# Optimization experiments

Hardware: AMD Instinct MI355X
Metric: run time of the kernel (lower is better)

Reference implementation:

```python
import jax, jax.numpy as jnp
import numpy as np

B = 1048576          # batch size
ALPHA1, ALPHA2, ALPHA3 = 1.2566, 1.5, 0.9
S_STAR = 20.0
TAU = 4.0


def _f_matrix(a1, a2, a3):
    # fixed 6x6 dynamics matrix built by the i in {1,2} loop in CBF_Parameters
    f = jnp.zeros((6, 6), jnp.float32)
    f = f.at[2, 1].set(1.0).at[2, 3].set(-1.0)
    f = f.at[3, 1].set(a3).at[3, 2].set(a1).at[3, 3].set(-a2)
    f = f.at[4, 3].set(1.0).at[4, 5].set(-1.0)
    f = f.at[5, 3].set(a3).at[5, 4].set(a1).at[5, 5].set(-a2)
    return f


def setup_inputs() -> dict:
    key = jax.random.key(0)
    ks = jax.random.split(key, 7)
    z = jax.random.normal(ks[0], (B, 6), jnp.float32)
    tilde_vh = jnp.zeros((1,), jnp.float32)  # unused in forward (dead code in source)
    W1 = jax.random.normal(ks[1], (50, 6), jnp.float32) * 0.3
    b1 = jax.random.normal(ks[2], (50,), jnp.float32) * 0.1
    W2 = jax.random.normal(ks[3], (100, 50), jnp.float32) * 0.1
    b2 = jax.random.normal(ks[4], (100,), jnp.float32) * 0.1
    W3 = jax.random.normal(ks[5], (5, 100), jnp.float32) * 0.1
    b3 = jax.random.normal(ks[6], (5,), jnp.float32) * 0.1
    return dict(z=z, tilde_vh=tilde_vh, W1=W1, b1=b1, W2=W2, b2=b2, W3=W3, b3=b3)


def reference(z, tilde_vh, W1, b1, W2, b2, W3, b3):
    # tiny MLP, no activations (faithful to fc3(fc2(fc1(z))))
    u = ((z @ W1.T + b1) @ W2.T + b2) @ W3.T + b3        # (B, 5)
    p1, p2, p3 = u[:, 1], u[:, 2], u[:, 3]

    # faithful: torch reshape (row-major reinterpret), not transpose
    X = z.reshape(6, -1)                                  # (6, B)
    f = _f_matrix(ALPHA1, ALPHA2, ALPHA3)
    fX = f @ X                                            # (6, B)

    # index == 2 constraint (while loop body never runs: delta_b[1]=tau != 0)
    d2 = jnp.zeros(6, jnp.float32).at[1].set(TAU).at[2].set(1.0).at[3].set(-TAU)
    eta1 = X[2] + S_STAR - TAU * (X[3] - X[1])            # (B,)
    bb1 = d2 @ fX + p1 * eta1                             # (B,)

    # index == 3 constraint (while loop runs exactly once: d3[1]==0 -> d3u[1]=tau*alpha3)
    d3 = jnp.zeros(6, jnp.float32).at[3].set(TAU).at[4].set(1.0).at[5].set(-TAU)
    d3u = d3 @ f                                          # one f-multiplication
    eta2a = X[4] + S_STAR - TAU * (X[5] - X[3])           # (B,)
    eta2b = d3u @ X                                       # (B,)
    bb2 = d3u @ fX + p2 * eta2a + p3 * eta2b              # (B,)

    A = jnp.stack([-d2[1], -d3u[1]])                      # (2,) constraint normals
    h = jnp.stack([bb1, bb2], axis=1)                     # (B, 2)

    # per-sample 1-D QP: min 0.25*x^2 - u0*x  s.t. A_i * x <= h_i  (Q = 0.5)
    x_unc = 2.0 * u[:, 0]
    ratios = h / A                                        # (B, 2)
    neg_inf = jnp.float32(-1e30)
    pos_inf = jnp.float32(1e30)
    lb = jnp.max(jnp.where(A < 0, ratios, neg_inf), axis=1)
    ub = jnp.min(jnp.where(A > 0, ratios, pos_inf), axis=1)
    return jnp.clip(x_unc, lb, ub)[:, None]               # (B, 1)
```

## Files before the change

### kernel.cpp

```cpp
#include <hip/hip_runtime.h>

#define ALPHA1 1.2566f
#define ALPHA2 1.5f
#define ALPHA3 0.9f
#define S_STAR 20.0f
#define TAU    4.0f

constexpr int TPB = 256;
constexpr int JPT = 2;
constexpr int JPB = TPB * JPT;

typedef float f32x4 __attribute__((ext_vector_type(4)));
typedef float f32x2 __attribute__((ext_vector_type(2)));

__device__ __forceinline__ f32x4 ntload4(const float* p) {
    return __builtin_nontemporal_load((const f32x4*)p);
}
__device__ __forceinline__ f32x2 ntload2(const float* p) {
    return __builtin_nontemporal_load((const f32x2*)p);
}

__global__ __launch_bounds__(TPB, 8) void fused_kernel(
        const float* __restrict__ z,
        const float* __restrict__ W1, const float* __restrict__ b1,
        const float* __restrict__ W2, const float* __restrict__ b2,
        const float* __restrict__ W3, const float* __restrict__ b3,
        float* __restrict__ out, long long B) {
    __shared__ float W1e[50][8];
    __shared__ float T[100][8];
    __shared__ float Mc[4][8];

    const int tid = threadIdx.x;
    const long long j0 = ((long long)blockIdx.x * TPB + tid) * JPT;

    const f32x4 r0 = ntload4(z + j0 * 6);
    const f32x4 r1 = ntload4(z + j0 * 6 + 4);
    const f32x4 r2 = ntload4(z + j0 * 6 + 8);
    const f32x2 c1 = ntload2(z + 1 * B + j0);
    const f32x2 c2 = ntload2(z + 2 * B + j0);
    const f32x2 c3 = ntload2(z + 3 * B + j0);
    const f32x2 c4 = ntload2(z + 4 * B + j0);
    const f32x2 c5 = ntload2(z + 5 * B + j0);

    if (tid < 50) {
        const float2 a = *(const float2*)(W1 + tid * 6);
        const float2 b = *(const float2*)(W1 + tid * 6 + 2);
        const float2 d = *(const float2*)(W1 + tid * 6 + 4);
        W1e[tid][0] = a.x; W1e[tid][1] = a.y;
        W1e[tid][2] = b.x; W1e[tid][3] = b.y;
        W1e[tid][4] = d.x; W1e[tid][5] = d.y;
        W1e[tid][6] = b1[tid];
    }
    __syncthreads();

    if (tid < 100) {
        float acc[7] = {0.f, 0.f, 0.f, 0.f, 0.f, 0.f, 0.f};
        acc[6] = b2[tid];
        const float2* wrow = (const float2*)(W2 + tid * 50);
        #pragma unroll 5
        for (int hh = 0; hh < 25; ++hh) {
            const float2 w = wrow[hh];
            const int h = 2 * hh;
            #pragma unroll
            for (int k = 0; k < 7; ++k)
                acc[k] = fmaf(w.y, W1e[h + 1][k], fmaf(w.x, W1e[h][k], acc[k]));
        }
        #pragma unroll
        for (int k = 0; k < 7; ++k) T[tid][k] = acc[k];
    }
    __syncthreads();

    if (tid < 28) {
        const int m = tid / 7, k = tid % 7;
        float s = (k == 6) ? b3[m] : 0.f;
        #pragma unroll 10
        for (int i = 0; i < 100; ++i)
            s = fmaf(W3[m * 100 + i], T[i][k], s);
        Mc[m][k] = s;
    }
    __syncthreads();

    const float g1 = TAU * ALPHA3;
    const float g2 = TAU * ALPHA1;
    const float g3 = 1.f - TAU * ALPHA2 - TAU * ALPHA3;
    const float g4 = -TAU * ALPHA1;
    const float g5 = TAU * ALPHA2 - 1.f;
    const float invA1 = -0.25f;
    const float invA2 = -1.f / (TAU * ALPHA3);

    const float zz[12] = {r0.x, r0.y, r0.z, r0.w,
                          r1.x, r1.y, r1.z, r1.w,
                          r2.x, r2.y, r2.z, r2.w};

    f32x2 o;
    #pragma unroll
    for (int r = 0; r < 2; ++r) {
        float u[4];
        #pragma unroll
        for (int m = 0; m < 4; ++m) {
            float s = Mc[m][6];
            #pragma unroll
            for (int k = 0; k < 6; ++k)
                s = fmaf(Mc[m][k], zz[r * 6 + k], s);
            u[m] = s;
        }
        const float x1 = r ? c1.y : c1.x;
        const float x2 = r ? c2.y : c2.x;
        const float x3 = r ? c3.y : c3.x;
        const float x4 = r ? c4.y : c4.x;
        const float x5 = r ? c5.y : c5.x;

        const float fx2 = x1 - x3;
        const float fx3 = ALPHA3 * x1 + ALPHA1 * x2 - ALPHA2 * x3;
        const float fx4 = x3 - x5;
        const float fx5 = ALPHA3 * x3 + ALPHA1 * x4 - ALPHA2 * x5;

        const float eta1 = x2 + S_STAR - TAU * (x3 - x1);
        const float bb1  = (fx2 - TAU * fx3) + u[1] * eta1;

        const float eta2a = x4 + S_STAR - TAU * (x5 - x3);
        const float eta2b = g1 * x1 + g2 * x2 + g3 * x3 + g4 * x4 + g5 * x5;
        const float d3ufX = g2 * fx2 + g3 * fx3 + g4 * fx4 + g5 * fx5;
        const float bb2   = d3ufX + u[2] * eta2a + u[3] * eta2b;

        const float lb = fmaxf(bb1 * invA1, bb2 * invA2);
        const float xu = 2.f * u[0];
        o[r] = fminf(fmaxf(xu, lb), 1e30f);
    }
    __builtin_nontemporal_store(o, (f32x2*)(out + j0));
}

extern "C" void kernel_launch(void* const* d_in, const int* in_sizes, int n_in,
                              void* d_out, int out_size, void* d_ws, size_t ws_size,
                              hipStream_t stream) {
    const float* z  = (const float*)d_in[0];
    const float* W1 = (const float*)d_in[2];
    const float* b1 = (const float*)d_in[3];
    const float* W2 = (const float*)d_in[4];
    const float* b2 = (const float*)d_in[5];
    const float* W3 = (const float*)d_in[6];
    const float* b3 = (const float*)d_in[7];
    float* out = (float*)d_out;

    const long long B = (long long)in_sizes[0] / 6;
    const int blocks = (int)(B / JPB);

    fused_kernel<<<blocks, TPB, 0, stream>>>(z, W1, b1, W2, b2, W3, b3, out, B);
}
```

Before: 105.9 us.

## Drop W1 LDS staging barrier, prefetch W3/b3 to LDS, use regular loads

Removes the first shared-memory staging of W1/b1 and its barrier; threads building the composite weights now read W1 and b1 directly from global memory (uniform addresses, likely scalar loads). Otherwise idle threads preload W3 and b3 into LDS in parallel, so the third-stage reduction reads from LDS instead of global memory. Non-temporal loads and stores of z and out are replaced with ordinary vector accesses, and the column loads are reordered before the row loads. Trade-off: each of the 100 threads reads W1 from global or cache instead of LDS, and cache policy changes for the streaming traffic.

```diff
diff --git a/kernel.cpp b/kernel.cpp
--- a/kernel.cpp
+++ b/kernel.cpp
@@ -13,45 +13,35 @@
 typedef float f32x4 __attribute__((ext_vector_type(4)));
 typedef float f32x2 __attribute__((ext_vector_type(2)));
 
-__device__ __forceinline__ f32x4 ntload4(const float* p) {
-    return __builtin_nontemporal_load((const f32x4*)p);
-}
-__device__ __forceinline__ f32x2 ntload2(const float* p) {
-    return __builtin_nontemporal_load((const f32x2*)p);
-}
-
 __global__ __launch_bounds__(TPB, 8) void fused_kernel(
         const float* __restrict__ z,
         const float* __restrict__ W1, const float* __restrict__ b1,
         const float* __restrict__ W2, const float* __restrict__ b2,
         const float* __restrict__ W3, const float* __restrict__ b3,
         float* __restrict__ out, long long B) {
-    __shared__ float W1e[50][8];
     __shared__ float T[100][8];
+    __shared__ float W3s[400];
+    __shared__ float b3s[4];
     __shared__ float Mc[4][8];
 
     const int tid = threadIdx.x;
     const long long j0 = ((long long)blockIdx.x * TPB + tid) * JPT;
 
-    const f32x4 r0 = ntload4(z + j0 * 6);
-    const f32x4 r1 = ntload4(z + j0 * 6 + 4);
-    const f32x4 r2 = ntload4(z + j0 * 6 + 8);
-    const f32x2 c1 = ntload2(z + 1 * B + j0);
-    const f32x2 c2 = ntload2(z + 2 * B + j0);
-    const f32x2 c3 = ntload2(z + 3 * B + j0);
-    const f32x2 c4 = ntload2(z + 4 * B + j0);
-    const f32x2 c5 = ntload2(z + 5 * B + j0);
+    const f32x2 c1 = *(const f32x2*)(z + 1 * B + j0);
+    const f32x2 c2 = *(const f32x2*)(z + 2 * B + j0);
+    const f32x2 c3 = *(const f32x2*)(z + 3 * B + j0);
+    const f32x2 c4 = *(const f32x2*)(z + 4 * B + j0);
+    const f32x2 c5 = *(const f32x2*)(z + 5 * B + j0);
+    const f32x4 r0 = *(const f32x4*)(z + j0 * 6);
+    const f32x4 r1 = *(const f32x4*)(z + j0 * 6 + 4);
+    const f32x4 r2 = *(const f32x4*)(z + j0 * 6 + 8);
 
-    if (tid < 50) {
-        const float2 a = *(const float2*)(W1 + tid * 6);
-        const float2 b = *(const float2*)(W1 + tid * 6 + 2);
-        const float2 d = *(const float2*)(W1 + tid * 6 + 4);
-        W1e[tid][0] = a.x; W1e[tid][1] = a.y;
-        W1e[tid][2] = b.x; W1e[tid][3] = b.y;
-        W1e[tid][4] = d.x; W1e[tid][5] = d.y;
-        W1e[tid][6] = b1[tid];
+    if (tid >= 128 && tid < 228) {
+        const int i = tid - 128;
+        *(f32x4*)(&W3s[i * 4]) = *(const f32x4*)(W3 + i * 4);
+    } else if (tid >= 228 && tid < 232) {
+        b3s[tid - 228] = b3[tid - 228];
     }
-    __syncthreads();
 
     if (tid < 100) {
         float acc[7] = {0.f, 0.f, 0.f, 0.f, 0.f, 0.f, 0.f};
@@ -62,8 +52,10 @@
             const float2 w = wrow[hh];
             const int h = 2 * hh;
             #pragma unroll
-            for (int k = 0; k < 7; ++k)
-                acc[k] = fmaf(w.y, W1e[h + 1][k], fmaf(w.x, W1e[h][k], acc[k]));
+            for (int k = 0; k < 6; ++k)
+                acc[k] = fmaf(w.y, W1[(h + 1) * 6 + k],
+                          fmaf(w.x, W1[h * 6 + k], acc[k]));
+            acc[6] = fmaf(w.y, b1[h + 1], fmaf(w.x, b1[h], acc[6]));
         }
         #pragma unroll
         for (int k = 0; k < 7; ++k) T[tid][k] = acc[k];
@@ -72,10 +64,10 @@
 
     if (tid < 28) {
         const int m = tid / 7, k = tid % 7;
-        float s = (k == 6) ? b3[m] : 0.f;
+        float s = (k == 6) ? b3s[m] : 0.f;
         #pragma unroll 10
         for (int i = 0; i < 100; ++i)
-            s = fmaf(W3[m * 100 + i], T[i][k], s);
+            s = fmaf(W3s[m * 100 + i], T[i][k], s);
         Mc[m][k] = s;
     }
     __syncthreads();
@@ -127,7 +119,7 @@
         const float xu = 2.f * u[0];
         o[r] = fminf(fmaxf(xu, lb), 1e30f);
     }
-    __builtin_nontemporal_store(o, (f32x2*)(out + j0));
+    *(f32x2*)(out + j0) = o;
 }
 
 extern "C" void kernel_launch(void* const* d_in, const int* in_sizes, int n_in,
```

Result: faster. 92.43 us (-12.8%).
